# Kernel optimization log

Measured on AMD Instinct MI355X. Metric: run time of the kernel, lower is better.

The kernel has to match this reference:

```python
import jax, jax.numpy as jnp
import numpy as np

B, T, E, H = 64, 512, 512, 64
NEG_INF = jnp.float32(-1e30)


def setup_inputs() -> dict:
    key = jax.random.key(0)
    kx, kk, kq, kv = jax.random.split(key, 4)
    x = jax.random.normal(kx, (B, T, E), dtype=jnp.float32)
    attn_mask = jnp.ones((B, T), dtype=jnp.int32)
    Wk = jax.random.normal(kk, (E, H), dtype=jnp.float32) * (E ** -0.5)
    Wq = jax.random.normal(kq, (E, H), dtype=jnp.float32) * (E ** -0.5)
    Wv = jax.random.normal(kv, (E, H), dtype=jnp.float32) * (E ** -0.5)
    return {"x": x, "attn_mask": attn_mask, "Wk": Wk, "Wq": Wq, "Wv": Wv}


def reference(x, attn_mask, Wk, Wq, Wv):
    # x: (B,T,E); projections to (B,T,H)
    k = x @ Wk
    q = x @ Wq
    v = x @ Wv
    # scaled attention scores (B,T,T)
    wei = jnp.einsum('bth,bsh->bts', q, k) * (H ** -0.5)
    t = x.shape[1]
    causal = jnp.tril(jnp.ones((t, t), dtype=bool))  # (T,T)
    wei = jnp.where(causal[None, :, :], wei, NEG_INF)
    # padding mask: attn_mask (B,T) broadcast over query dim (matches unsqueeze(1).expand)
    wei = jnp.where(attn_mask[:, None, :] != 0, wei, NEG_INF)
    wei = jax.nn.softmax(wei, axis=-1)
    # dropout omitted (eval mode) for deterministic correctness baseline
    return jnp.einsum('bts,bsh->bth', wei, v)
```

## Files before the change

kernel.cpp:

```cpp
#include <hip/hip_runtime.h>

#define B 64
#define T 512
#define E 512
#define H 64
#define NEG_INF (-1e30f)

#define PBM 64
#define PBK 64
#define PN 192
#define NCHK (E / PBK)

#define QSCALE 0.18033688011112043f
#define DEFER_THR 8.0f

using short8 = __attribute__((ext_vector_type(8))) short;
using f32x16 = __attribute__((ext_vector_type(16))) float;

__device__ __forceinline__ unsigned short f2bf(float f) {
    unsigned int u = __float_as_uint(f);
    u += 0x7fffu + ((u >> 16) & 1u);
    return (unsigned short)(u >> 16);
}
__device__ __forceinline__ unsigned int bfpack_tr(float lo, float hi) {
    return (__float_as_uint(hi) & 0xffff0000u) | (__float_as_uint(lo) >> 16);
}
__device__ __forceinline__ void async_copy16(const void* g, void* l) {
    __builtin_amdgcn_global_load_lds(
        (const __attribute__((address_space(1))) unsigned int*)g,
        (__attribute__((address_space(3))) unsigned int*)l, 16, 0, 0);
}

__global__ __launch_bounds__(256) void prep(
    const float* __restrict__ Wq, const float* __restrict__ Wk,
    const float* __restrict__ Wv, const int* __restrict__ am,
    unsigned short* __restrict__ WT_swz, unsigned int* __restrict__ mbits)
{
    const int bid = blockIdx.x;
    if (bid < 384) {
        const int i = bid * 256 + threadIdx.x;
        const int c   = i / (PN * 64);
        const int rem = i - c * (PN * 64);
        const int row = rem >> 6;
        const int s   = rem & 63;
        const int klocal = s ^ ((row & 7) << 3);
        const int k   = c * 64 + klocal;
        const int seg = row >> 6, hh = row & 63;
        const float* W = (seg == 0) ? Wq : (seg == 1) ? Wk : Wv;
        WT_swz[i] = f2bf(W[(size_t)k * H + hh]);
    } else {
        const int i = (bid - 384) * 256 + threadIdx.x;
        const unsigned long long bal = __ballot(am[i] != 0);
        const int lane = threadIdx.x & 63;
        if (lane == 0)       mbits[i >> 5] = (unsigned int)bal;
        else if (lane == 32) mbits[i >> 5] = (unsigned int)(bal >> 32);
    }
}

__global__ __launch_bounds__(256) void proj_gemm(
    const float* __restrict__ x,
    const unsigned short* __restrict__ WT_swz,
    unsigned short* __restrict__ qfrag, unsigned short* __restrict__ kfrag,
    unsigned short* __restrict__ vfrag)
{
    __shared__ unsigned short Xs[2][PBM * 64];
    __shared__ unsigned short Ws[2][PN * 64];

    const int tid  = threadIdx.x;
    const int wid  = tid >> 6;
    const int lane = tid & 63;
    const int hi   = lane >> 5;
    const int r    = lane & 31;
    const int row0 = blockIdx.x * PBM;

    const int mrow  = (wid >> 1) * 32 + r;
    const int cbase = (wid & 1) * 96;

    const int aBase = mrow * 128;
    const int aXor  = (mrow & 7) << 4;
    int bBase[3], bXor[3];
    #pragma unroll
    for (int nt = 0; nt < 3; ++nt) {
        const int col = cbase + nt * 32 + r;
        bBase[nt] = col * 128;
        bXor[nt]  = (col & 7) << 4;
    }
    const int xs_rr[2]  = { tid >> 3, (256 + tid) >> 3 };
    const int xs_s16[2] = { tid & 7, tid & 7 };

    f32x16 acc[3] = {};

    {
        #pragma unroll
        for (int p = 0; p < 6; ++p) {
            const int u = p * 256 + wid * 64 + lane;
            async_copy16(WT_swz + u * 8, (char*)(&Ws[0][0]) + (p * 256 + wid * 64) * 16);
        }
        #pragma unroll
        for (int p = 0; p < 2; ++p) {
            const int rr = xs_rr[p], s16 = xs_s16[p];
            const float4* src = reinterpret_cast<const float4*>(
                &x[(size_t)(row0 + rr) * E + s16 * 8]);
            const float4 a0 = src[0], a1 = src[1];
            union { unsigned short us[8]; short8 v; } pk;
            pk.us[0] = f2bf(a0.x); pk.us[1] = f2bf(a0.y);
            pk.us[2] = f2bf(a0.z); pk.us[3] = f2bf(a0.w);
            pk.us[4] = f2bf(a1.x); pk.us[5] = f2bf(a1.y);
            pk.us[6] = f2bf(a1.z); pk.us[7] = f2bf(a1.w);
            const int cb = (s16 * 16) ^ ((rr & 7) << 4);
            *reinterpret_cast<short8*>((char*)(&Xs[0][0]) + rr * 128 + cb) = pk.v;
        }
        __syncthreads();
    }

    for (int c = 0; c < NCHK; ++c) {
        const int cur = c & 1;
        const bool pre = (c + 1 < NCHK);
        float4 xa[2], xb[2];

        if (pre) {
            const unsigned short* gw = WT_swz + (size_t)(c + 1) * (PN * 64);
            #pragma unroll
            for (int p = 0; p < 6; ++p) {
                const int u = p * 256 + wid * 64 + lane;
                async_copy16(gw + u * 8,
                             (char*)(&Ws[cur ^ 1][0]) + (p * 256 + wid * 64) * 16);
            }
            const int kc = (c + 1) * PBK;
            #pragma unroll
            for (int p = 0; p < 2; ++p) {
                const float4* src = reinterpret_cast<const float4*>(
                    &x[(size_t)(row0 + xs_rr[p]) * E + kc + xs_s16[p] * 8]);
                xa[p] = src[0];
                xb[p] = src[1];
            }
        }

        #pragma unroll
        for (int ks = 0; ks < 4; ++ks) {
            const int koff = ks * 32 + hi * 16;
            const short8 a = *reinterpret_cast<const short8*>(
                (const char*)(&Xs[cur][0]) + aBase + (koff ^ aXor));
            #pragma unroll
            for (int nt = 0; nt < 3; ++nt) {
                const short8 b = *reinterpret_cast<const short8*>(
                    (const char*)(&Ws[cur][0]) + bBase[nt] + (koff ^ bXor[nt]));
                acc[nt] = __builtin_amdgcn_mfma_f32_32x32x16_bf16(a, b, acc[nt], 0, 0, 0);
            }
        }

        if (pre) {
            #pragma unroll
            for (int p = 0; p < 2; ++p) {
                const int rr = xs_rr[p], s16 = xs_s16[p];
                union { unsigned short us[8]; short8 v; } pk;
                pk.us[0] = f2bf(xa[p].x); pk.us[1] = f2bf(xa[p].y);
                pk.us[2] = f2bf(xa[p].z); pk.us[3] = f2bf(xa[p].w);
                pk.us[4] = f2bf(xb[p].x); pk.us[5] = f2bf(xb[p].y);
                pk.us[6] = f2bf(xb[p].z); pk.us[7] = f2bf(xb[p].w);
                const int cb = (s16 * 16) ^ ((rr & 7) << 4);
                *reinterpret_cast<short8*>((char*)(&Xs[cur ^ 1][0]) + rr * 128 + cb) = pk.v;
            }
        }
        __syncthreads();
    }

    #pragma unroll
    for (int nt = 0; nt < 3; ++nt) {
        const int gc  = cbase + nt * 32 + r;
        const int seg = gc >> 6;
        const int h   = gc & 63;
        #pragma unroll
        for (int reg = 0; reg < 16; ++reg) {
            const int drow = (reg & 3) + 8 * (reg >> 2) + 4 * hi;
            const int grow = row0 + (wid >> 1) * 32 + drow;
            const float val = acc[nt][reg];
            const int bb  = grow >> 9;
            const int key = grow & 511;
            const int blk = key >> 5;
            const int kk  = key & 31;
            if (seg == 0) {
                qfrag[(((size_t)bb * 16 + blk) * 4 + (h >> 4)) * 512
                      + (((h >> 3) & 1) * 32 + kk) * 8 + (h & 7)] = f2bf(val * QSCALE);
            } else if (seg == 1) {
                kfrag[(((size_t)bb * 16 + blk) * 4 + (h >> 4)) * 512
                      + (((h >> 3) & 1) * 32 + kk) * 8 + (h & 7)] = f2bf(val);
            } else {
                vfrag[(((size_t)bb * 16 + blk) * 4 + ((kk >> 4) * 2 + (h >> 5))) * 512
                      + (((kk >> 3) & 1) * 32 + (h & 31)) * 8 + (kk & 7)] = f2bf(val);
            }
        }
    }
}

__global__ __launch_bounds__(64) void attn_online(
    const unsigned short* __restrict__ qfrag,
    const unsigned short* __restrict__ kfrag,
    const unsigned short* __restrict__ vfrag,
    const unsigned int* __restrict__ mbits,
    float* __restrict__ out)
{
    const int lane = threadIdx.x;
    const int hi = lane >> 5, r = lane & 31;
    const int h4 = 4 * hi;

    const int bid = blockIdx.x;
    const int k   = bid >> 3;
    const int b   = ((k >> 4) << 3) | (bid & 7);
    const int s   = 15 - (k & 15);
    const int t0  = s * 32;
    const int tq  = t0 + r;

    const int l8 = lane * 8;

    short8 qf[4];
    {
        const unsigned short* qb = qfrag + (((size_t)b * 16 + s) * 4) * 512;
        #pragma unroll
        for (int ks = 0; ks < 4; ++ks)
            qf[ks] = *reinterpret_cast<const short8*>(qb + ks * 512 + l8);
    }

    f32x16 accO[2] = {};
    float m = -INFINITY, l = 0.f;

    short8 kf[4], vb[4];
    {
        const unsigned short* kb = kfrag + ((size_t)b * 16) * 4 * 512;
        const unsigned short* vv = vfrag + ((size_t)b * 16) * 4 * 512;
        #pragma unroll
        for (int ks = 0; ks < 4; ++ks) {
            kf[ks] = *reinterpret_cast<const short8*>(kb + ks * 512 + l8);
            vb[ks] = *reinterpret_cast<const short8*>(vv + ks * 512 + l8);
        }
    }

    for (int j = 0; j <= s; ++j) {
        short8 kn[4], vn[4];
        if (j < s) {
            const unsigned short* kb = kfrag + (((size_t)b * 16 + j + 1) * 4) * 512;
            const unsigned short* vv = vfrag + (((size_t)b * 16 + j + 1) * 4) * 512;
            #pragma unroll
            for (int ks = 0; ks < 4; ++ks) {
                kn[ks] = *reinterpret_cast<const short8*>(kb + ks * 512 + l8);
                vn[ks] = *reinterpret_cast<const short8*>(vv + ks * 512 + l8);
            }
        }

        f32x16 sc = {};
        #pragma unroll
        for (int ks = 0; ks < 4; ++ks)
            sc = __builtin_amdgcn_mfma_f32_32x32x16_bf16(kf[ks], qf[ks], sc, 0, 0, 0);

        const unsigned int mw = mbits[b * 16 + j];
        float cmax = -INFINITY;
        if (j == s) {
            #pragma unroll
            for (int reg = 0; reg < 16; ++reg) {
                const int cr = (reg & 3) + 8 * (reg >> 2) + h4;
                float v = sc[reg];
                const bool bad = !((mw >> cr) & 1u) || (32 * j + cr > tq);
                v = bad ? NEG_INF : v;
                sc[reg] = v;
                cmax = fmaxf(cmax, v);
            }
        } else {
            #pragma unroll
            for (int reg = 0; reg < 16; ++reg) {
                const int cr = (reg & 3) + 8 * (reg >> 2) + h4;
                float v = sc[reg];
                v = ((mw >> cr) & 1u) ? v : NEG_INF;
                sc[reg] = v;
                cmax = fmaxf(cmax, v);
            }
        }
        cmax = fmaxf(cmax, __shfl_xor(cmax, 32));

        if (!__all(cmax <= m + DEFER_THR)) {
            const float m_new = fmaxf(m, cmax);
            const float scale = exp2f(m - m_new);
            f32x16 scf;
            #pragma unroll
            for (int reg = 0; reg < 16; ++reg)
                scf[reg] = __shfl(scale, (reg & 3) + 8 * (reg >> 2) + h4);
            #pragma unroll
            for (int reg = 0; reg < 16; ++reg) {
                accO[0][reg] *= scf[reg];
                accO[1][reg] *= scf[reg];
            }
            l *= scale;
            m = m_new;
        }

        float csum = 0.f;
        #pragma unroll
        for (int reg = 0; reg < 16; ++reg) {
            const float p = exp2f(sc[reg] - m);
            sc[reg] = p;
            csum += p;
        }
        csum += __shfl_xor(csum, 32);
        l += csum;

        unsigned int pk[8];
        #pragma unroll
        for (int jj = 0; jj < 8; ++jj)
            pk[jj] = bfpack_tr(sc[2 * jj], sc[2 * jj + 1]);
        #pragma unroll
        for (int hs = 0; hs < 2; ++hs) {
            const unsigned int p01 = pk[hs * 4 + 0], p23 = pk[hs * 4 + 1];
            const unsigned int p45 = pk[hs * 4 + 2], p67 = pk[hs * 4 + 3];
            const unsigned int sendA = hi ? p01 : p45;
            const unsigned int sendB = hi ? p23 : p67;
            const unsigned int recvA = (unsigned int)__shfl_xor((int)sendA, 32);
            const unsigned int recvB = (unsigned int)__shfl_xor((int)sendB, 32);
            union { unsigned int uu[4]; short8 s8; } aw;
            aw.uu[0] = hi ? recvA : p01;
            aw.uu[1] = hi ? recvB : p23;
            aw.uu[2] = hi ? p45 : recvA;
            aw.uu[3] = hi ? p67 : recvB;
            #pragma unroll
            for (int tile = 0; tile < 2; ++tile)
                accO[tile] = __builtin_amdgcn_mfma_f32_32x32x16_bf16(
                    aw.s8, vb[hs * 2 + tile], accO[tile], 0, 0, 0);
        }

        #pragma unroll
        for (int ks = 0; ks < 4; ++ks) { kf[ks] = kn[ks]; vb[ks] = vn[ks]; }
    }

    const float inv = 1.f / l;
    #pragma unroll
    for (int reg = 0; reg < 16; ++reg) {
        const int qrow = (reg & 3) + 8 * (reg >> 2) + h4;
        const float f = __shfl(inv, qrow);
        float* op = &out[((size_t)b * T + t0 + qrow) * H];
        op[r]      = accO[0][reg] * f;
        op[r + 32] = accO[1][reg] * f;
    }
}

extern "C" void kernel_launch(void* const* d_in, const int* in_sizes, int n_in,
                              void* d_out, int out_size, void* d_ws, size_t ws_size,
                              hipStream_t stream) {
    const float* x         = (const float*)d_in[0];
    const int*   attn_mask = (const int*)d_in[1];
    const float* Wk        = (const float*)d_in[2];
    const float* Wq        = (const float*)d_in[3];
    const float* Wv        = (const float*)d_in[4];
    float* out = (float*)d_out;

    unsigned short* qfrag  = (unsigned short*)d_ws;
    unsigned short* kfrag  = qfrag + (size_t)B * T * H;
    unsigned short* vfrag  = kfrag + (size_t)B * T * H;
    unsigned short* WT_swz = vfrag + (size_t)B * T * H;
    unsigned int*   mbits  = (unsigned int*)(WT_swz + (size_t)PN * E);

    prep<<<512, 256, 0, stream>>>(Wq, Wk, Wv, attn_mask, WT_swz, mbits);
    proj_gemm<<<(B * T) / PBM, 256, 0, stream>>>(x, WT_swz, qfrag, kfrag, vfrag);
    attn_online<<<B * 16, 64, 0, stream>>>(qfrag, kfrag, vfrag, mbits, out);
}
```

Measured before the change: 54.01 us.

## Load full x tile to LDS once and read MFMA-fragment weights from global

The projection GEMM no longer streams x and weights through double-buffered LDS chunks. It loads the whole 64x512 x tile as bf16 into 64KB of LDS with a rotation swizzle and a single barrier. The weights are pre-laid out by prep in MFMA fragment order, so each lane reads B operands straight from global/L2. The Q scale is also folded into the weights in prep. This removes the per-chunk barriers and the weight LDS traffic, but the larger LDS footprint can cut occupancy and there is little overlap between the x load and compute.

After: 58.71 us. 1.09x slower.

```diff
diff --git a/kernel.cpp b/kernel.cpp
--- a/kernel.cpp
+++ b/kernel.cpp
@@ -7,9 +7,7 @@
 #define NEG_INF (-1e30f)
 
 #define PBM 64
-#define PBK 64
 #define PN 192
-#define NCHK (E / PBK)
 
 #define QSCALE 0.18033688011112043f
 #define DEFER_THR 8.0f
@@ -25,29 +23,29 @@
 __device__ __forceinline__ unsigned int bfpack_tr(float lo, float hi) {
     return (__float_as_uint(hi) & 0xffff0000u) | (__float_as_uint(lo) >> 16);
 }
-__device__ __forceinline__ void async_copy16(const void* g, void* l) {
-    __builtin_amdgcn_global_load_lds(
-        (const __attribute__((address_space(1))) unsigned int*)g,
-        (__attribute__((address_space(3))) unsigned int*)l, 16, 0, 0);
-}
 
 __global__ __launch_bounds__(256) void prep(
     const float* __restrict__ Wq, const float* __restrict__ Wk,
     const float* __restrict__ Wv, const int* __restrict__ am,
-    unsigned short* __restrict__ WT_swz, unsigned int* __restrict__ mbits)
+    unsigned short* __restrict__ wfrag, unsigned int* __restrict__ mbits)
 {
     const int bid = blockIdx.x;
     if (bid < 384) {
-        const int i = bid * 256 + threadIdx.x;
-        const int c   = i / (PN * 64);
-        const int rem = i - c * (PN * 64);
-        const int row = rem >> 6;
-        const int s   = rem & 63;
-        const int klocal = s ^ ((row & 7) << 3);
-        const int k   = c * 64 + klocal;
-        const int seg = row >> 6, hh = row & 63;
+        const int i  = bid * 256 + threadIdx.x;
+        const int f  = i >> 9;
+        const int le = i & 511;
+        const int ln = le >> 3, e = le & 7;
+        const int ko = ln >> 5, rr = ln & 31;
+        const int c  = f / 24;
+        const int ks = (f - c * 24) / 6;
+        const int ct = f % 6;
+        const int col = ct * 32 + rr;
+        const int kk  = c * 64 + ks * 16 + ko * 8 + e;
+        const int seg = col >> 6, hh = col & 63;
         const float* W = (seg == 0) ? Wq : (seg == 1) ? Wk : Wv;
-        WT_swz[i] = f2bf(W[(size_t)k * H + hh]);
+        float v = W[(size_t)kk * H + hh];
+        if (seg == 0) v *= QSCALE;
+        wfrag[i] = f2bf(v);
     } else {
         const int i = (bid - 384) * 256 + threadIdx.x;
         const unsigned long long bal = __ballot(am[i] != 0);
@@ -59,12 +57,11 @@
 
 __global__ __launch_bounds__(256) void proj_gemm(
     const float* __restrict__ x,
-    const unsigned short* __restrict__ WT_swz,
+    const unsigned short* __restrict__ wfrag,
     unsigned short* __restrict__ qfrag, unsigned short* __restrict__ kfrag,
     unsigned short* __restrict__ vfrag)
 {
-    __shared__ unsigned short Xs[2][PBM * 64];
-    __shared__ unsigned short Ws[2][PN * 64];
+    __shared__ unsigned short Xs[PBM * 512];
 
     const int tid  = threadIdx.x;
     const int wid  = tid >> 6;
@@ -73,101 +70,57 @@
     const int r    = lane & 31;
     const int row0 = blockIdx.x * PBM;
 
-    const int mrow  = (wid >> 1) * 32 + r;
-    const int cbase = (wid & 1) * 96;
-
-    const int aBase = mrow * 128;
-    const int aXor  = (mrow & 7) << 4;
-    int bBase[3], bXor[3];
+    #pragma unroll
+    for (int half = 0; half < 2; ++half) {
+        float4 va[8], vb2[8];
+        #pragma unroll
+        for (int p = 0; p < 8; ++p) {
+            const int i  = (half * 8 + p) * 256 + tid;
+            const int rr = i >> 6, g = i & 63;
+            const float4* src = reinterpret_cast<const float4*>(
+                &x[(size_t)(row0 + rr) * E + g * 8]);
+            va[p]  = src[0];
+            vb2[p] = src[1];
+        }
+        #pragma unroll
+        for (int p = 0; p < 8; ++p) {
+            const int i  = (half * 8 + p) * 256 + tid;
+            const int rr = i >> 6, g = i & 63;
+            union { unsigned short us[8]; short8 v; } pk;
+            pk.us[0] = f2bf(va[p].x);  pk.us[1] = f2bf(va[p].y);
+            pk.us[2] = f2bf(va[p].z);  pk.us[3] = f2bf(va[p].w);
+            pk.us[4] = f2bf(vb2[p].x); pk.us[5] = f2bf(vb2[p].y);
+            pk.us[6] = f2bf(vb2[p].z); pk.us[7] = f2bf(vb2[p].w);
+            *reinterpret_cast<short8*>(
+                (char*)Xs + rr * 1024 + ((g + rr) & 63) * 16) = pk.v;
+        }
+    }
+    __syncthreads();
+
+    const int mrow = (wid >> 1) * 32 + r;
+    const int ctb  = (wid & 1) * 3;
+    f32x16 acc[3] = {};
+
+    #pragma unroll
+    for (int c = 0; c < 8; ++c) {
+        #pragma unroll
+        for (int ks = 0; ks < 4; ++ks) {
+            const int g = c * 8 + ks * 2 + hi;
+            const short8 a = *reinterpret_cast<const short8*>(
+                (const char*)Xs + mrow * 1024 + ((g + mrow) & 63) * 16);
+            #pragma unroll
+            for (int nt = 0; nt < 3; ++nt) {
+                const int f = (c * 4 + ks) * 6 + ctb + nt;
+                const short8 b = *reinterpret_cast<const short8*>(
+                    wfrag + (size_t)f * 512 + lane * 8);
+                acc[nt] = __builtin_amdgcn_mfma_f32_32x32x16_bf16(a, b, acc[nt], 0, 0, 0);
+            }
+        }
+    }
+
     #pragma unroll
     for (int nt = 0; nt < 3; ++nt) {
-        const int col = cbase + nt * 32 + r;
-        bBase[nt] = col * 128;
-        bXor[nt]  = (col & 7) << 4;
-    }
-    const int xs_rr[2]  = { tid >> 3, (256 + tid) >> 3 };
-    const int xs_s16[2] = { tid & 7, tid & 7 };
-
-    f32x16 acc[3] = {};
-
-    {
-        #pragma unroll
-        for (int p = 0; p < 6; ++p) {
-            const int u = p * 256 + wid * 64 + lane;
-            async_copy16(WT_swz + u * 8, (char*)(&Ws[0][0]) + (p * 256 + wid * 64) * 16);
-        }
-        #pragma unroll
-        for (int p = 0; p < 2; ++p) {
-            const int rr = xs_rr[p], s16 = xs_s16[p];
-            const float4* src = reinterpret_cast<const float4*>(
-                &x[(size_t)(row0 + rr) * E + s16 * 8]);
-            const float4 a0 = src[0], a1 = src[1];
-            union { unsigned short us[8]; short8 v; } pk;
-            pk.us[0] = f2bf(a0.x); pk.us[1] = f2bf(a0.y);
-            pk.us[2] = f2bf(a0.z); pk.us[3] = f2bf(a0.w);
-            pk.us[4] = f2bf(a1.x); pk.us[5] = f2bf(a1.y);
-            pk.us[6] = f2bf(a1.z); pk.us[7] = f2bf(a1.w);
-            const int cb = (s16 * 16) ^ ((rr & 7) << 4);
-            *reinterpret_cast<short8*>((char*)(&Xs[0][0]) + rr * 128 + cb) = pk.v;
-        }
-        __syncthreads();
-    }
-
-    for (int c = 0; c < NCHK; ++c) {
-        const int cur = c & 1;
-        const bool pre = (c + 1 < NCHK);
-        float4 xa[2], xb[2];
-
-        if (pre) {
-            const unsigned short* gw = WT_swz + (size_t)(c + 1) * (PN * 64);
-            #pragma unroll
-            for (int p = 0; p < 6; ++p) {
-                const int u = p * 256 + wid * 64 + lane;
-                async_copy16(gw + u * 8,
-                             (char*)(&Ws[cur ^ 1][0]) + (p * 256 + wid * 64) * 16);
-            }
-            const int kc = (c + 1) * PBK;
-            #pragma unroll
-            for (int p = 0; p < 2; ++p) {
-                const float4* src = reinterpret_cast<const float4*>(
-                    &x[(size_t)(row0 + xs_rr[p]) * E + kc + xs_s16[p] * 8]);
-                xa[p] = src[0];
-                xb[p] = src[1];
-            }
-        }
-
-        #pragma unroll
-        for (int ks = 0; ks < 4; ++ks) {
-            const int koff = ks * 32 + hi * 16;
-            const short8 a = *reinterpret_cast<const short8*>(
-                (const char*)(&Xs[cur][0]) + aBase + (koff ^ aXor));
-            #pragma unroll
-            for (int nt = 0; nt < 3; ++nt) {
-                const short8 b = *reinterpret_cast<const short8*>(
-                    (const char*)(&Ws[cur][0]) + bBase[nt] + (koff ^ bXor[nt]));
-                acc[nt] = __builtin_amdgcn_mfma_f32_32x32x16_bf16(a, b, acc[nt], 0, 0, 0);
-            }
-        }
-
-        if (pre) {
-            #pragma unroll
-            for (int p = 0; p < 2; ++p) {
-                const int rr = xs_rr[p], s16 = xs_s16[p];
-                union { unsigned short us[8]; short8 v; } pk;
-                pk.us[0] = f2bf(xa[p].x); pk.us[1] = f2bf(xa[p].y);
-                pk.us[2] = f2bf(xa[p].z); pk.us[3] = f2bf(xa[p].w);
-                pk.us[4] = f2bf(xb[p].x); pk.us[5] = f2bf(xb[p].y);
-                pk.us[6] = f2bf(xb[p].z); pk.us[7] = f2bf(xb[p].w);
-                const int cb = (s16 * 16) ^ ((rr & 7) << 4);
-                *reinterpret_cast<short8*>((char*)(&Xs[cur ^ 1][0]) + rr * 128 + cb) = pk.v;
-            }
-        }
-        __syncthreads();
-    }
-
-    #pragma unroll
-    for (int nt = 0; nt < 3; ++nt) {
-        const int gc  = cbase + nt * 32 + r;
+        const int gc  = (ctb + nt) * 32 + r;
         const int seg = gc >> 6;
         const int h   = gc & 63;
         #pragma unroll
@@ -181,7 +134,7 @@
             const int kk  = key & 31;
             if (seg == 0) {
                 qfrag[(((size_t)bb * 16 + blk) * 4 + (h >> 4)) * 512
-                      + (((h >> 3) & 1) * 32 + kk) * 8 + (h & 7)] = f2bf(val * QSCALE);
+                      + (((h >> 3) & 1) * 32 + kk) * 8 + (h & 7)] = f2bf(val);
             } else if (seg == 1) {
                 kfrag[(((size_t)bb * 16 + blk) * 4 + (h >> 4)) * 512
                       + (((h >> 3) & 1) * 32 + kk) * 8 + (h & 7)] = f2bf(val);
@@ -350,13 +303,13 @@
     const float* Wv        = (const float*)d_in[4];
     float* out = (float*)d_out;
 
-    unsigned short* qfrag  = (unsigned short*)d_ws;
-    unsigned short* kfrag  = qfrag + (size_t)B * T * H;
-    unsigned short* vfrag  = kfrag + (size_t)B * T * H;
-    unsigned short* WT_swz = vfrag + (size_t)B * T * H;
-    unsigned int*   mbits  = (unsigned int*)(WT_swz + (size_t)PN * E);
-
-    prep<<<512, 256, 0, stream>>>(Wq, Wk, Wv, attn_mask, WT_swz, mbits);
-    proj_gemm<<<(B * T) / PBM, 256, 0, stream>>>(x, WT_swz, qfrag, kfrag, vfrag);
+    unsigned short* qfrag = (unsigned short*)d_ws;
+    unsigned short* kfrag = qfrag + (size_t)B * T * H;
+    unsigned short* vfrag = kfrag + (size_t)B * T * H;
+    unsigned short* wfrag = vfrag + (size_t)B * T * H;
+    unsigned int*   mbits = (unsigned int*)(wfrag + (size_t)PN * E);
+
+    prep<<<512, 256, 0, stream>>>(Wq, Wk, Wv, attn_mask, wfrag, mbits);
+    proj_gemm<<<(B * T) / PBM, 256, 0, stream>>>(x, wfrag, qfrag, kfrag, vfrag);
     attn_online<<<B * 16, 64, 0, stream>>>(qfrag, kfrag, vfrag, mbits, out);
 }
```

## Split attention key blocks across four waves with LDS softmax merge

Applied to the files above, without the earlier changes.

The attention kernel goes from one wave per 32-query tile to four waves, each taking every fourth key block (split-K flash attention). Partial max, sum and output tiles go to shared memory and are combined with a log-sum-exp rescale before a vectorised store. A fast path also skips mask selects for fully unmasked key blocks. This shortens the serial chain for tiles with many key blocks, at the cost of more threads, LDS traffic, a barrier and idle waves on short tiles.

Measured after the change: 48.13 us. -10.9%, faster.

```diff
diff --git a/kernel.cpp b/kernel.cpp
--- a/kernel.cpp
+++ b/kernel.cpp
@@ -193,150 +193,197 @@
     }
 }
 
-__global__ __launch_bounds__(64) void attn_online(
+__global__ __launch_bounds__(256) void attn_online(
     const unsigned short* __restrict__ qfrag,
     const unsigned short* __restrict__ kfrag,
     const unsigned short* __restrict__ vfrag,
     const unsigned int* __restrict__ mbits,
     float* __restrict__ out)
 {
-    const int lane = threadIdx.x;
+    __shared__ float mlS[4][2][32];
+    __shared__ float Ob[4][32][68];
+
+    const int tid  = threadIdx.x;
+    const int w    = tid >> 6;
+    const int lane = tid & 63;
     const int hi = lane >> 5, r = lane & 31;
     const int h4 = 4 * hi;
 
     const int bid = blockIdx.x;
-    const int k   = bid >> 3;
-    const int b   = ((k >> 4) << 3) | (bid & 7);
-    const int s   = 15 - (k & 15);
+    const int kk2 = bid >> 3;
+    const int b   = ((kk2 >> 4) << 3) | (bid & 7);
+    const int s   = 15 - (kk2 & 15);
     const int t0  = s * 32;
     const int tq  = t0 + r;
-
-    const int l8 = lane * 8;
-
-    short8 qf[4];
-    {
-        const unsigned short* qb = qfrag + (((size_t)b * 16 + s) * 4) * 512;
-        #pragma unroll
-        for (int ks = 0; ks < 4; ++ks)
-            qf[ks] = *reinterpret_cast<const short8*>(qb + ks * 512 + l8);
-    }
+    const int l8  = lane * 8;
 
     f32x16 accO[2] = {};
     float m = -INFINITY, l = 0.f;
 
-    short8 kf[4], vb[4];
-    {
-        const unsigned short* kb = kfrag + ((size_t)b * 16) * 4 * 512;
-        const unsigned short* vv = vfrag + ((size_t)b * 16) * 4 * 512;
-        #pragma unroll
-        for (int ks = 0; ks < 4; ++ks) {
-            kf[ks] = *reinterpret_cast<const short8*>(kb + ks * 512 + l8);
-            vb[ks] = *reinterpret_cast<const short8*>(vv + ks * 512 + l8);
-        }
-    }
-
-    for (int j = 0; j <= s; ++j) {
-        short8 kn[4], vn[4];
-        if (j < s) {
-            const unsigned short* kb = kfrag + (((size_t)b * 16 + j + 1) * 4) * 512;
-            const unsigned short* vv = vfrag + (((size_t)b * 16 + j + 1) * 4) * 512;
+    if (w <= s) {
+        short8 qf[4];
+        {
+            const unsigned short* qb = qfrag + (((size_t)b * 16 + s) * 4) * 512;
+            #pragma unroll
+            for (int ks = 0; ks < 4; ++ks)
+                qf[ks] = *reinterpret_cast<const short8*>(qb + ks * 512 + l8);
+        }
+        short8 kf[4], vb[4];
+        {
+            const unsigned short* kb = kfrag + (((size_t)b * 16 + w) * 4) * 512;
+            const unsigned short* vv = vfrag + (((size_t)b * 16 + w) * 4) * 512;
             #pragma unroll
             for (int ks = 0; ks < 4; ++ks) {
-                kn[ks] = *reinterpret_cast<const short8*>(kb + ks * 512 + l8);
-                vn[ks] = *reinterpret_cast<const short8*>(vv + ks * 512 + l8);
-            }
-        }
-
-        f32x16 sc = {};
-        #pragma unroll
-        for (int ks = 0; ks < 4; ++ks)
-            sc = __builtin_amdgcn_mfma_f32_32x32x16_bf16(kf[ks], qf[ks], sc, 0, 0, 0);
-
-        const unsigned int mw = mbits[b * 16 + j];
-        float cmax = -INFINITY;
-        if (j == s) {
+                kf[ks] = *reinterpret_cast<const short8*>(kb + ks * 512 + l8);
+                vb[ks] = *reinterpret_cast<const short8*>(vv + ks * 512 + l8);
+            }
+        }
+
+        for (int j = w; j <= s; j += 4) {
+            short8 kn[4], vn[4];
+            if (j + 4 <= s) {
+                const unsigned short* kb = kfrag + (((size_t)b * 16 + j + 4) * 4) * 512;
+                const unsigned short* vv = vfrag + (((size_t)b * 16 + j + 4) * 4) * 512;
+                #pragma unroll
+                for (int ks = 0; ks < 4; ++ks) {
+                    kn[ks] = *reinterpret_cast<const short8*>(kb + ks * 512 + l8);
+                    vn[ks] = *reinterpret_cast<const short8*>(vv + ks * 512 + l8);
+                }
+            }
+
+            f32x16 sc = {};
+            #pragma unroll
+            for (int ks = 0; ks < 4; ++ks)
+                sc = __builtin_amdgcn_mfma_f32_32x32x16_bf16(kf[ks], qf[ks], sc, 0, 0, 0);
+
+            const unsigned int mw = mbits[b * 16 + j];
+            const bool fullm = (mw == 0xffffffffu);
+            float cmax = -INFINITY;
+            if (j == s) {
+                #pragma unroll
+                for (int reg = 0; reg < 16; ++reg) {
+                    const int cr = (reg & 3) + 8 * (reg >> 2) + h4;
+                    float v = sc[reg];
+                    const bool bad = (32 * j + cr > tq) || (!fullm && !((mw >> cr) & 1u));
+                    v = bad ? NEG_INF : v;
+                    sc[reg] = v;
+                    cmax = fmaxf(cmax, v);
+                }
+            } else if (fullm) {
+                #pragma unroll
+                for (int reg = 0; reg < 16; ++reg)
+                    cmax = fmaxf(cmax, sc[reg]);
+            } else {
+                #pragma unroll
+                for (int reg = 0; reg < 16; ++reg) {
+                    const int cr = (reg & 3) + 8 * (reg >> 2) + h4;
+                    float v = sc[reg];
+                    v = ((mw >> cr) & 1u) ? v : NEG_INF;
+                    sc[reg] = v;
+                    cmax = fmaxf(cmax, v);
+                }
+            }
+            cmax = fmaxf(cmax, __shfl_xor(cmax, 32));
+
+            if (!__all(cmax <= m + DEFER_THR)) {
+                const float m_new = fmaxf(m, cmax);
+                const float scale = exp2f(m - m_new);
+                f32x16 scf;
+                #pragma unroll
+                for (int reg = 0; reg < 16; ++reg)
+                    scf[reg] = __shfl(scale, (reg & 3) + 8 * (reg >> 2) + h4);
+                #pragma unroll
+                for (int reg = 0; reg < 16; ++reg) {
+                    accO[0][reg] *= scf[reg];
+                    accO[1][reg] *= scf[reg];
+                }
+                l *= scale;
+                m = m_new;
+            }
+
+            float csum = 0.f;
             #pragma unroll
             for (int reg = 0; reg < 16; ++reg) {
-                const int cr = (reg & 3) + 8 * (reg >> 2) + h4;
-                float v = sc[reg];
-                const bool bad = !((mw >> cr) & 1u) || (32 * j + cr > tq);
-                v = bad ? NEG_INF : v;
-                sc[reg] = v;
-                cmax = fmaxf(cmax, v);
-            }
-        } else {
-            #pragma unroll
-            for (int reg = 0; reg < 16; ++reg) {
-                const int cr = (reg & 3) + 8 * (reg >> 2) + h4;
-                float v = sc[reg];
-                v = ((mw >> cr) & 1u) ? v : NEG_INF;
-                sc[reg] = v;
-                cmax = fmaxf(cmax, v);
-            }
-        }
-        cmax = fmaxf(cmax, __shfl_xor(cmax, 32));
-
-        if (!__all(cmax <= m + DEFER_THR)) {
-            const float m_new = fmaxf(m, cmax);
-            const float scale = exp2f(m - m_new);
-            f32x16 scf;
-            #pragma unroll
-            for (int reg = 0; reg < 16; ++reg)
-                scf[reg] = __shfl(scale, (reg & 3) + 8 * (reg >> 2) + h4);
-            #pragma unroll
-            for (int reg = 0; reg < 16; ++reg) {
-                accO[0][reg] *= scf[reg];
-                accO[1][reg] *= scf[reg];
-            }
-            l *= scale;
-            m = m_new;
-        }
-
-        float csum = 0.f;
-        #pragma unroll
-        for (int reg = 0; reg < 16; ++reg) {
-            const float p = exp2f(sc[reg] - m);
-            sc[reg] = p;
-            csum += p;
-        }
-        csum += __shfl_xor(csum, 32);
-        l += csum;
-
-        unsigned int pk[8];
-        #pragma unroll
-        for (int jj = 0; jj < 8; ++jj)
-            pk[jj] = bfpack_tr(sc[2 * jj], sc[2 * jj + 1]);
-        #pragma unroll
-        for (int hs = 0; hs < 2; ++hs) {
-            const unsigned int p01 = pk[hs * 4 + 0], p23 = pk[hs * 4 + 1];
-            const unsigned int p45 = pk[hs * 4 + 2], p67 = pk[hs * 4 + 3];
-            const unsigned int sendA = hi ? p01 : p45;
-            const unsigned int sendB = hi ? p23 : p67;
-            const unsigned int recvA = (unsigned int)__shfl_xor((int)sendA, 32);
-            const unsigned int recvB = (unsigned int)__shfl_xor((int)sendB, 32);
-            union { unsigned int uu[4]; short8 s8; } aw;
-            aw.uu[0] = hi ? recvA : p01;
-            aw.uu[1] = hi ? recvB : p23;
-            aw.uu[2] = hi ? p45 : recvA;
-            aw.uu[3] = hi ? p67 : recvB;
-            #pragma unroll
-            for (int tile = 0; tile < 2; ++tile)
-                accO[tile] = __builtin_amdgcn_mfma_f32_32x32x16_bf16(
-                    aw.s8, vb[hs * 2 + tile], accO[tile], 0, 0, 0);
-        }
-
-        #pragma unroll
-        for (int ks = 0; ks < 4; ++ks) { kf[ks] = kn[ks]; vb[ks] = vn[ks]; }
-    }
-
-    const float inv = 1.f / l;
+                const float p = exp2f(sc[reg] - m);
+                sc[reg] = p;
+                csum += p;
+            }
+            csum += __shfl_xor(csum, 32);
+            l += csum;
+
+            unsigned int pk[8];
+            #pragma unroll
+            for (int jj = 0; jj < 8; ++jj)
+                pk[jj] = bfpack_tr(sc[2 * jj], sc[2 * jj + 1]);
+            #pragma unroll
+            for (int hs = 0; hs < 2; ++hs) {
+                const unsigned int p01 = pk[hs * 4 + 0], p23 = pk[hs * 4 + 1];
+                const unsigned int p45 = pk[hs * 4 + 2], p67 = pk[hs * 4 + 3];
+                const unsigned int sendA = hi ? p01 : p45;
+                const unsigned int sendB = hi ? p23 : p67;
+                const unsigned int recvA = (unsigned int)__shfl_xor((int)sendA, 32);
+                const unsigned int recvB = (unsigned int)__shfl_xor((int)sendB, 32);
+                union { unsigned int uu[4]; short8 s8; } aw;
+                aw.uu[0] = hi ? recvA : p01;
+                aw.uu[1] = hi ? recvB : p23;
+                aw.uu[2] = hi ? p45 : recvA;
+                aw.uu[3] = hi ? p67 : recvB;
+                #pragma unroll
+                for (int tile = 0; tile < 2; ++tile)
+                    accO[tile] = __builtin_amdgcn_mfma_f32_32x32x16_bf16(
+                        aw.s8, vb[hs * 2 + tile], accO[tile], 0, 0, 0);
+            }
+
+            #pragma unroll
+            for (int ks = 0; ks < 4; ++ks) { kf[ks] = kn[ks]; vb[ks] = vn[ks]; }
+        }
+    }
+
+    if (hi == 0) { mlS[w][0][r] = m; mlS[w][1][r] = l; }
     #pragma unroll
     for (int reg = 0; reg < 16; ++reg) {
         const int qrow = (reg & 3) + 8 * (reg >> 2) + h4;
-        const float f = __shfl(inv, qrow);
-        float* op = &out[((size_t)b * T + t0 + qrow) * H];
-        op[r]      = accO[0][reg] * f;
-        op[r + 32] = accO[1][reg] * f;
+        Ob[w][qrow][r]      = accO[0][reg];
+        Ob[w][qrow][r + 32] = accO[1][reg];
+    }
+    __syncthreads();
+
+    {
+        const int row = tid >> 3;
+        const int c8  = (tid & 7) * 8;
+
+        float mi[4], li[4];
+        float mstar = -INFINITY;
+        #pragma unroll
+        for (int w2 = 0; w2 < 4; ++w2) {
+            mi[w2] = mlS[w2][0][row];
+            li[w2] = mlS[w2][1][row];
+            mstar = fmaxf(mstar, mi[w2]);
+        }
+        float L = 0.f, fw[4];
+        #pragma unroll
+        for (int w2 = 0; w2 < 4; ++w2) {
+            fw[w2] = exp2f(mi[w2] - mstar);
+            L += fw[w2] * li[w2];
+        }
+        const float inv = 1.f / L;
+
+        float acc[8] = {};
+        #pragma unroll
+        for (int w2 = 0; w2 < 4; ++w2) {
+            const float4 lo = *reinterpret_cast<const float4*>(&Ob[w2][row][c8]);
+            const float4 hi4v = *reinterpret_cast<const float4*>(&Ob[w2][row][c8 + 4]);
+            acc[0] += fw[w2] * lo.x;  acc[1] += fw[w2] * lo.y;
+            acc[2] += fw[w2] * lo.z;  acc[3] += fw[w2] * lo.w;
+            acc[4] += fw[w2] * hi4v.x; acc[5] += fw[w2] * hi4v.y;
+            acc[6] += fw[w2] * hi4v.z; acc[7] += fw[w2] * hi4v.w;
+        }
+
+        float* op = &out[((size_t)b * T + t0 + row) * H + c8];
+        float4 o0 = { acc[0] * inv, acc[1] * inv, acc[2] * inv, acc[3] * inv };
+        float4 o1 = { acc[4] * inv, acc[5] * inv, acc[6] * inv, acc[7] * inv };
+        *reinterpret_cast<float4*>(op)     = o0;
+        *reinterpret_cast<float4*>(op + 4) = o1;
     }
 }
 
@@ -358,5 +405,5 @@
 
     prep<<<512, 256, 0, stream>>>(Wq, Wk, Wv, attn_mask, WT_swz, mbits);
     proj_gemm<<<(B * T) / PBM, 256, 0, stream>>>(x, WT_swz, qfrag, kfrag, vfrag);
-    attn_online<<<B * 16, 64, 0, stream>>>(qfrag, kfrag, vfrag, mbits, out);
-}
+    attn_online<<<B * 16, 256, 0, stream>>>(qfrag, kfrag, vfrag, mbits, out);
+}
```
